# Kernel optimization log

Measured on AMD Instinct MI355X. Metric: run time of the kernel, lower is better.

The kernel has to match this reference:

```python
import jax, jax.numpy as jnp
import numpy as np

N_NODES = 40000
N_EDGES = 640000
IN, HID, OUT = 128, 128, 47


def setup_inputs() -> dict:
    key = jax.random.key(0)
    ks = jax.random.split(key, 12)
    def glorot(k, shape):
        fan = sum(shape)
        return jax.random.normal(k, shape, dtype=jnp.float32) * jnp.sqrt(2.0 / fan)
    return {
        "x": jax.random.normal(ks[0], (N_NODES, IN), dtype=jnp.float32),
        "src": jax.random.randint(ks[1], (N_EDGES,), 0, N_NODES),
        "dst": jax.random.randint(ks[2], (N_EDGES,), 0, N_NODES),
        "W_self0": glorot(ks[3], (IN, HID)),
        "W_neigh0": glorot(ks[4], (IN, HID)),
        "b0": jnp.zeros((HID,), dtype=jnp.float32),
        "W_self1": glorot(ks[5], (HID, HID)),
        "W_neigh1": glorot(ks[6], (HID, HID)),
        "b1": jnp.zeros((HID,), dtype=jnp.float32),
        "W_self2": glorot(ks[7], (HID, OUT)),
        "W_neigh2": glorot(ks[8], (HID, OUT)),
        "b2": jnp.zeros((OUT,), dtype=jnp.float32),
    }


def _sage_conv(h, src, dst, W_self, W_neigh, b):
    # DGL SAGEConv('mean'): mean of neighbor (src) feats scattered to dst,
    # then fc_neigh(h_neigh) + fc_self(h_self) + bias.
    n = h.shape[0]
    deg = jax.ops.segment_sum(jnp.ones_like(dst, dtype=h.dtype), dst, num_segments=n)
    agg = jax.ops.segment_sum(h[src], dst, num_segments=n)          # [N, d] gather + scatter-add
    h_neigh = agg / jnp.maximum(deg, 1.0)[:, None]                   # isolated nodes -> 0 (DGL behavior)
    return h @ W_self + h_neigh @ W_neigh + b


def reference(x, src, dst, W_self0, W_neigh0, b0, W_self1, W_neigh1, b1,
              W_self2, W_neigh2, b2):
    # Dropout is identity in eval mode; omitted here.
    h = _sage_conv(x, src, dst, W_self0, W_neigh0, b0)
    h = jax.nn.relu(h)
    h = _sage_conv(h, src, dst, W_self1, W_neigh1, b1)
    h = jax.nn.relu(h)
    h = _sage_conv(h, src, dst, W_self2, W_neigh2, b2)
    return h
```

## Files before the change

### kernel.cpp

```cpp
#include <hip/hip_runtime.h>
#include <hip/hip_bf16.h>
#include <stdint.h>

#define NN 40000
#define NE 640000
#define NB 157

typedef __attribute__((ext_vector_type(8))) short bf16x8;
typedef __attribute__((ext_vector_type(4))) float f32x4;
typedef __attribute__((ext_vector_type(2))) float f32x2v;

static __device__ __forceinline__ unsigned short f2b(float f) {
    unsigned b = __float_as_uint(f);
    return (unsigned short)((b + 0x7FFFu + ((b >> 16) & 1u)) >> 16);
}
static __device__ __forceinline__ float blo(unsigned v) { return __uint_as_float(v << 16); }
static __device__ __forceinline__ float bhi(unsigned v) { return __uint_as_float(v & 0xffff0000u); }

static __device__ __forceinline__ void acc4(float* a, uint2 v) {
    a[0] += blo(v.x); a[1] += bhi(v.x);
    a[2] += blo(v.y); a[3] += bhi(v.y);
}


#if __has_builtin(__builtin_amdgcn_cvt_pk_fp8_f32) && __has_builtin(__builtin_amdgcn_cvt_pk_f32_fp8)
#define FP8_HW 1
#else
#define FP8_HW 0
#endif

static __device__ __forceinline__ unsigned char f2fp8_sw(float f) {
    f = fminf(fmaxf(f, -448.f), 448.f);
    unsigned b = __float_as_uint(f);
    unsigned s = (b >> 24) & 0x80u;
    unsigned ab = b & 0x7fffffffu;
    if (ab < 0x3c000000u) return (unsigned char)s;
    unsigned r = ab + 0x7ffffu + ((ab >> 20) & 1u);
    unsigned e = ((r >> 23) - 120u) & 0xfu;
    unsigned m = (r >> 20) & 7u;
    return (unsigned char)(s | (e << 3) | m);
}
static __device__ __forceinline__ float fp82f_sw(unsigned char u) {
    unsigned s = ((unsigned)u & 0x80u) << 24;
    unsigned e = (u >> 3) & 15u, m = u & 7u;
    float nrm = __uint_as_float(s | ((e + 120u) << 23) | (m << 20));
    float dnm = __uint_as_float(s | 0x3f800000u) * (float)m * 0.001953125f;
    return e ? nrm : dnm;
}

static __device__ __forceinline__ unsigned pack_fp8x4(float a, float b, float c, float d) {
#if FP8_HW
    int v = __builtin_amdgcn_cvt_pk_fp8_f32(a, b, 0, false);
    v = __builtin_amdgcn_cvt_pk_fp8_f32(c, d, v, true);
    return (unsigned)v;
#else
    return (unsigned)f2fp8_sw(a) | ((unsigned)f2fp8_sw(b) << 8) |
           ((unsigned)f2fp8_sw(c) << 16) | ((unsigned)f2fp8_sw(d) << 24);
#endif
}

static __device__ __forceinline__ void acc4f8(float* a, unsigned v) {
#if FP8_HW
    f32x2v p0 = __builtin_amdgcn_cvt_pk_f32_fp8((int)v, false);
    f32x2v p1 = __builtin_amdgcn_cvt_pk_f32_fp8((int)v, true);
    a[0] += p0.x; a[1] += p0.y; a[2] += p1.x; a[3] += p1.y;
#else
    a[0] += fp82f_sw(v & 0xff);         a[1] += fp82f_sw((v >> 8) & 0xff);
    a[2] += fp82f_sw((v >> 16) & 0xff); a[3] += fp82f_sw(v >> 24);
#endif
}
static __device__ __forceinline__ void acc16f8(float* a, uint4 v) {
    acc4f8(a, v.x); acc4f8(a + 4, v.y); acc4f8(a + 8, v.z); acc4f8(a + 12, v.w);
}


__global__ __launch_bounds__(256) void scan1_kernel(const int* __restrict__ deg,
                                                    int* __restrict__ bsum) {
    int i = blockIdx.x * 256 + threadIdx.x;
    int v = (i < NN) ? deg[i] : 0;
#pragma unroll
    for (int off = 1; off < 64; off <<= 1) v += __shfl_xor(v, off);
    __shared__ int ws4[4];
    if ((threadIdx.x & 63) == 0) ws4[threadIdx.x >> 6] = v;
    __syncthreads();
    if (threadIdx.x == 0) bsum[blockIdx.x] = ws4[0] + ws4[1] + ws4[2] + ws4[3];
}

__global__ void scan_top_kernel(const int* __restrict__ bsum, int* __restrict__ btop) {
    int lane = threadIdx.x;
    int run = 0;
    for (int base = 0; base < NB; base += 64) {
        int idx = base + lane;
        int v = (idx < NB) ? bsum[idx] : 0;
        int s = v;
#pragma unroll
        for (int off = 1; off < 64; off <<= 1) { int t = __shfl_up(s, off); if (lane >= off) s += t; }
        if (idx < NB) btop[idx] = run + s - v;
        run += __shfl(s, 63);
    }
}

__global__ __launch_bounds__(256) void scan2_kernel(const int* __restrict__ deg,
                                                    const int* __restrict__ btop,
                                                    int* __restrict__ row_ptr) {
    int b = blockIdx.x;
    int i = b * 256 + threadIdx.x;
    int lane = threadIdx.x & 63, wv = threadIdx.x >> 6;
    int v = (i < NN) ? deg[i] : 0;
    int s = v;
#pragma unroll
    for (int off = 1; off < 64; off <<= 1) { int t = __shfl_up(s, off); if (lane >= off) s += t; }
    __shared__ int wsum[4];
    if (lane == 63) wsum[wv] = s;
    __syncthreads();
    int add = btop[b];
    for (int w = 0; w < wv; ++w) add += wsum[w];
    if (i < NN) row_ptr[i] = add + s - v;
    if (i == NN - 1) row_ptr[NN] = add + s;
}

__global__ void fill_csr_kernel(const int* __restrict__ src, const int* __restrict__ dst,
                                const int* __restrict__ row_ptr, int* __restrict__ cursor,
                                int* __restrict__ csr, int n) {
    int i = blockIdx.x * blockDim.x + threadIdx.x;
    if (i < n) {
        int d = dst[i];
        int pos = row_ptr[d] + atomicAdd(&cursor[d], 1);
        csr[pos] = src[i];
    }
}


__global__ __launch_bounds__(256) void prep_kernel(
    const float* __restrict__ x, const int* __restrict__ dst,
    const float* __restrict__ Ws0, const float* __restrict__ Wn0,
    const float* __restrict__ Ws1, const float* __restrict__ Wn1,
    const float* __restrict__ Ws2, const float* __restrict__ Wn2,
    int* __restrict__ deg, unsigned short* __restrict__ X,
    unsigned char* __restrict__ X8, unsigned char* __restrict__ H18,
    unsigned short* __restrict__ Hn,
    unsigned short* __restrict__ Wt0, unsigned short* __restrict__ Wt1,
    unsigned short* __restrict__ Wt2s, unsigned short* __restrict__ Wt2n) {
    int b = blockIdx.x, tid = threadIdx.x;
    if (b < 2500) {
        int i = b * 256 + tid;
        atomicAdd(&deg[dst[i]], 1);
    } else if (b < 7500) {
        int i = (b - 2500) * 256 + tid;
        int e = i << 2;
        float4 v = *(const float4*)(x + e);
        uint2 o;
        o.x = f2b(v.x) | ((unsigned)f2b(v.y) << 16);
        o.y = f2b(v.z) | ((unsigned)f2b(v.w) << 16);
        *(uint2*)(X + e) = o;
        *(unsigned*)(X8 + e) = pack_fp8x4(v.x, v.y, v.z, v.w);
    } else if (b < 7804) {
        int i = (b - 7500) * 256 + tid;
        if (i < 65536) {
            int l = i >> 15, j = i & 32767;
            int n = j >> 8, k = j & 255;
            const float* Ws = l ? Ws1 : Ws0;
            const float* Wn = l ? Wn1 : Wn0;
            float v = (k < 128) ? Ws[k * 128 + n] : Wn[(k - 128) * 128 + n];
            (l ? Wt1 : Wt0)[n * 256 + k] = f2b(v);
        } else if (i < 65536 + 6144) {
            int j = i - 65536;
            int n = j >> 7, k = j & 127;
            float v = (n < 47) ? Ws2[k * 47 + n] : 0.f;
            Wt2s[n * 128 + k] = f2b(v);
        } else {
            int j = i - 65536 - 6144;
            int n = j >> 7, k = j & 127;
            float v = (n < 47) ? Wn2[k * 47 + n] : 0.f;
            Wt2n[n * 128 + k] = f2b(v);
        }
    } else {
        if (tid < 16) *(uint2*)(X8 + (size_t)NN * 128 + tid * 8) = (uint2){0, 0};
        else if (tid < 32) *(uint2*)(H18 + (size_t)NN * 128 + (tid - 16) * 8) = (uint2){0, 0};
        else if (tid < 48) *(uint2*)((unsigned char*)(Hn + (size_t)NN * 64) + (tid - 32) * 8) = (uint2){0, 0};
    }
}


template <bool RELU, bool WFP8>
__global__ __launch_bounds__(256) void sage_layer_kernel(
    const unsigned short* __restrict__ Hin, const unsigned char* __restrict__ H8in,
    const int* __restrict__ csr, const int* __restrict__ row_ptr,
    const unsigned short* __restrict__ Wt, const float* __restrict__ bias,
    unsigned short* __restrict__ Hout, unsigned char* __restrict__ H8out) {
    __shared__ unsigned short agg_lds[16 * 128];

    int tid = threadIdx.x;
    int wv = tid >> 6, lane = tid & 63;
    int lr = lane & 15, lg = lane >> 4;
    int lr8 = lane & 7, g = lane >> 3;
    int t = g >> 1, sub = g & 1;
    int m0 = blockIdx.x * 16;

    bf16x8 afr[8];
#pragma unroll
    for (int kt = 0; kt < 4; ++kt)
        afr[kt] = *(const bf16x8*)(Hin + (size_t)(m0 + lr) * 128 + kt * 32 + lg * 8);

    int nb = m0 + wv * 4;
    int rp5 = (lane < 5) ? row_ptr[nb + lane] : 0;
    int beg = __shfl(rp5, t), end = __shfl(rp5, t + 1);
    int deg = end - beg;
    int half = (deg + 1) >> 1;
    int js = beg + sub * half;
    int je = sub ? end : beg + half;
    int last = (je > js) ? je - 1 : js;

    float a[16] = {};
    for (int j = js; j < je; j += 8) {
        int idxs[8];
#pragma unroll
        for (int k = 0; k < 8; ++k) idxs[k] = csr[min(j + k, last)];
#pragma unroll
        for (int k = 0; k < 8; ++k)
            if (j + k >= je) idxs[k] = NN;
        uint4 v[8];
#pragma unroll
        for (int k = 0; k < 8; ++k)
            v[k] = *(const uint4*)(H8in + (size_t)idxs[k] * 128 + lr8 * 16);
#pragma unroll
        for (int k = 0; k < 8; ++k) acc16f8(a, v[k]);
    }
#pragma unroll
    for (int k = 0; k < 16; ++k) a[k] += __shfl_xor(a[k], 8);

    if (sub == 0) {
        float inv = 1.0f / fmaxf((float)deg, 1.0f);
        uint4 o0, o1;
        o0.x = f2b(a[0] * inv)  | ((unsigned)f2b(a[1] * inv) << 16);
        o0.y = f2b(a[2] * inv)  | ((unsigned)f2b(a[3] * inv) << 16);
        o0.z = f2b(a[4] * inv)  | ((unsigned)f2b(a[5] * inv) << 16);
        o0.w = f2b(a[6] * inv)  | ((unsigned)f2b(a[7] * inv) << 16);
        o1.x = f2b(a[8] * inv)  | ((unsigned)f2b(a[9] * inv) << 16);
        o1.y = f2b(a[10] * inv) | ((unsigned)f2b(a[11] * inv) << 16);
        o1.z = f2b(a[12] * inv) | ((unsigned)f2b(a[13] * inv) << 16);
        o1.w = f2b(a[14] * inv) | ((unsigned)f2b(a[15] * inv) << 16);
        int row = wv * 4 + t;
        *(uint4*)&agg_lds[row * 128 + ((2 * lr8) ^ row) * 8] = o0;
        *(uint4*)&agg_lds[row * 128 + ((2 * lr8 + 1) ^ row) * 8] = o1;
    }
    __syncthreads();

#pragma unroll
    for (int kt = 0; kt < 4; ++kt) {
        int chunk = (kt * 4 + lg) ^ lr;
        afr[4 + kt] = *(const bf16x8*)&agg_lds[lr * 128 + chunk * 8];
    }

    int n0 = (wv * 2) * 16 + lr;
    int n1 = n0 + 16;
    f32x4 acc0 = (f32x4){0.f, 0.f, 0.f, 0.f};
    f32x4 acc1 = (f32x4){0.f, 0.f, 0.f, 0.f};
#pragma unroll
    for (int kt = 0; kt < 8; ++kt) {
        bf16x8 b0 = *(const bf16x8*)(Wt + (size_t)n0 * 256 + kt * 32 + lg * 8);
        bf16x8 b1 = *(const bf16x8*)(Wt + (size_t)n1 * 256 + kt * 32 + lg * 8);
        acc0 = __builtin_amdgcn_mfma_f32_16x16x32_bf16(afr[kt], b0, acc0, 0, 0, 0);
        acc1 = __builtin_amdgcn_mfma_f32_16x16x32_bf16(afr[kt], b1, acc1, 0, 0, 0);
    }

    float bs0 = bias[n0], bs1 = bias[n1];
#pragma unroll
    for (int r = 0; r < 4; ++r) {
        int m = m0 + lg * 4 + r;
        float v0 = acc0[r] + bs0;
        float v1 = acc1[r] + bs1;
        if (RELU) { v0 = fmaxf(v0, 0.f); v1 = fmaxf(v1, 0.f); }
        Hout[(size_t)m * 128 + n0] = f2b(v0);
        Hout[(size_t)m * 128 + n1] = f2b(v1);
        if (WFP8) {
#if FP8_HW
            H8out[(size_t)m * 128 + n0] =
                (unsigned char)(__builtin_amdgcn_cvt_pk_fp8_f32(v0, v0, 0, false) & 0xff);
            H8out[(size_t)m * 128 + n1] =
                (unsigned char)(__builtin_amdgcn_cvt_pk_fp8_f32(v1, v1, 0, false) & 0xff);
#else
            H8out[(size_t)m * 128 + n0] = f2fp8_sw(v0);
            H8out[(size_t)m * 128 + n1] = f2fp8_sw(v1);
#endif
        }
    }
}


__global__ __launch_bounds__(192) void dual_gemm_kernel(
    const unsigned short* __restrict__ H2,
    const unsigned short* __restrict__ Wt2s, const unsigned short* __restrict__ Wt2n,
    const float* __restrict__ b2,
    float* __restrict__ out, unsigned short* __restrict__ Hn) {
    int wv = threadIdx.x >> 6, lane = threadIdx.x & 63;
    int lr = lane & 15, lg = lane >> 4;

    bf16x8 bfr[2][4];
    float bs[2];
#pragma unroll
    for (int c = 0; c < 2; ++c) {
        int t = wv * 2 + c;
        bool is_s = t < 3;
        int n = (is_s ? t : t - 3) * 16 + lr;
        const unsigned short* W = is_s ? Wt2s : Wt2n;
#pragma unroll
        for (int kt = 0; kt < 4; ++kt)
            bfr[c][kt] = *(const bf16x8*)(W + (size_t)n * 128 + kt * 32 + lg * 8);
        bs[c] = (is_s && n < 47) ? b2[n] : 0.f;
    }

    for (int tt = 0; tt < 2; ++tt) {
        int m0 = blockIdx.x * 32 + tt * 16;
        bf16x8 afr[4];
#pragma unroll
        for (int kt = 0; kt < 4; ++kt)
            afr[kt] = *(const bf16x8*)(H2 + (size_t)(m0 + lr) * 128 + kt * 32 + lg * 8);
        f32x4 acc[2];
#pragma unroll
        for (int c = 0; c < 2; ++c) acc[c] = (f32x4){0.f, 0.f, 0.f, 0.f};
#pragma unroll
        for (int kt = 0; kt < 4; ++kt)
#pragma unroll
            for (int c = 0; c < 2; ++c)
                acc[c] = __builtin_amdgcn_mfma_f32_16x16x32_bf16(afr[kt], bfr[c][kt], acc[c], 0, 0, 0);
#pragma unroll
        for (int c = 0; c < 2; ++c) {
            int t = wv * 2 + c;
            bool is_s = t < 3;
            int n = (is_s ? t : t - 3) * 16 + lr;
#pragma unroll
            for (int r = 0; r < 4; ++r) {
                int m = m0 + lg * 4 + r;
                float v = acc[c][r] + bs[c];
                if (is_s) {
                    if (n < 47) out[(size_t)m * 47 + n] = v;
                } else {
                    Hn[(size_t)m * 64 + n] = f2b(v);
                }
            }
        }
    }
}


__global__ __launch_bounds__(256) void aggregate_out_kernel(
    const unsigned short* __restrict__ Hn, const int* __restrict__ csr,
    const int* __restrict__ row_ptr, float* __restrict__ out) {
    int wave = (blockIdx.x * blockDim.x + threadIdx.x) >> 6;
    int lane = threadIdx.x & 63;
    int nb = wave * 2;
    if (nb >= NN) return;
    int t = lane >> 5, sub = (lane >> 4) & 1, lc = lane & 15;
    int rp3 = (lane < 3) ? row_ptr[nb + lane] : 0;
    int beg = __shfl(rp3, t), end = __shfl(rp3, t + 1);
    int deg = end - beg;
    int half = (deg + 1) >> 1;
    int js = beg + sub * half;
    int je = sub ? end : beg + half;
    int last = (je > js) ? je - 1 : js;

    float a[4] = {};
    for (int j = js; j < je; j += 8) {
        int idxs[8];
#pragma unroll
        for (int k = 0; k < 8; ++k) idxs[k] = csr[min(j + k, last)];
#pragma unroll
        for (int k = 0; k < 8; ++k)
            if (j + k >= je) idxs[k] = NN;
        uint2 v[8];
#pragma unroll
        for (int k = 0; k < 8; ++k)
            v[k] = *(const uint2*)(Hn + (size_t)idxs[k] * 64 + lc * 4);
#pragma unroll
        for (int k = 0; k < 8; ++k) acc4(a, v[k]);
    }
#pragma unroll
    for (int k = 0; k < 4; ++k) a[k] += __shfl_xor(a[k], 16);

    if (sub == 0 && lc < 12) {
        float inv = 1.0f / fmaxf((float)deg, 1.0f);
        int node = nb + t;
        int c0 = lc * 4;
#pragma unroll
        for (int r = 0; r < 4; ++r)
            if (c0 + r < 47) out[(size_t)node * 47 + c0 + r] += a[r] * inv;
    }
}


extern "C" void kernel_launch(void* const* d_in, const int* in_sizes, int n_in,
                              void* d_out, int out_size, void* d_ws, size_t ws_size,
                              hipStream_t stream) {
    const float* x   = (const float*)d_in[0];
    const int*   src = (const int*)d_in[1];
    const int*   dst = (const int*)d_in[2];
    const float* Ws0 = (const float*)d_in[3];
    const float* Wn0 = (const float*)d_in[4];
    const float* b0  = (const float*)d_in[5];
    const float* Ws1 = (const float*)d_in[6];
    const float* Wn1 = (const float*)d_in[7];
    const float* b1  = (const float*)d_in[8];
    const float* Ws2 = (const float*)d_in[9];
    const float* Wn2 = (const float*)d_in[10];
    const float* b2  = (const float*)d_in[11];
    float* out = (float*)d_out;

    uintptr_t p = ((uintptr_t)d_ws + 255) & ~(uintptr_t)255;
    auto take = [&](size_t bytes) {
        void* r = (void*)p;
        p = (p + bytes + 255) & ~(uintptr_t)255;
        return r;
    };
    int* deg     = (int*)take(40000 * 4);
    int* cursor  = (int*)take(40000 * 4);
    int* row_ptr = (int*)take(40004 * 4);
    int* csr     = (int*)take(640000 * 4);
    unsigned short* X   = (unsigned short*)take((size_t)NN * 128 * 2);
    unsigned short* H1  = (unsigned short*)take((size_t)NN * 128 * 2);
    unsigned short* H2  = X;
    unsigned short* Wt0 = (unsigned short*)take(128 * 256 * 2);
    unsigned short* Wt1 = (unsigned short*)take(128 * 256 * 2);
    unsigned short* Wt2s = (unsigned short*)take(48 * 128 * 2);
    unsigned short* Wt2n = (unsigned short*)take(48 * 128 * 2);
    unsigned short* Hn  = (unsigned short*)take((size_t)(NN + 1) * 64 * 2);
    int* bsum = (int*)take(NB * 4);
    int* btop = (int*)take(NB * 4);
    unsigned char* X8  = (unsigned char*)take((size_t)(NN + 1) * 128);
    unsigned char* H18 = (unsigned char*)take((size_t)(NN + 1) * 128);

    hipMemsetAsync(deg, 0, 80000 * sizeof(int), stream);
    prep_kernel<<<7805, 256, 0, stream>>>(x, dst, Ws0, Wn0, Ws1, Wn1, Ws2, Wn2,
                                          deg, X, X8, H18, Hn, Wt0, Wt1, Wt2s, Wt2n);
    scan1_kernel<<<NB, 256, 0, stream>>>(deg, bsum);
    scan_top_kernel<<<1, 64, 0, stream>>>(bsum, btop);
    scan2_kernel<<<NB, 256, 0, stream>>>(deg, btop, row_ptr);
    fill_csr_kernel<<<2500, 256, 0, stream>>>(src, dst, row_ptr, cursor, csr, NE);

    sage_layer_kernel<true, true><<<2500, 256, 0, stream>>>(X, X8, csr, row_ptr, Wt0, b0, H1, H18);
    sage_layer_kernel<true, false><<<2500, 256, 0, stream>>>(H1, H18, csr, row_ptr, Wt1, b1, H2, nullptr);
    dual_gemm_kernel<<<1250, 192, 0, stream>>>(H2, Wt2s, Wt2n, b2, out, Hn);
    aggregate_out_kernel<<<5000, 256, 0, stream>>>(Hn, csr, row_ptr, out);
}
```

Measured before the change: 180.1 us.

## Split feature tables into column slabs and separate aggregation from GEMM

Stores the fp8 feature tables as two 64-column slabs and the final-layer neighbor projections as 32- and 16-column slabs. Aggregation runs in column-split passes so each gather pass works on a smaller table that fits better in cache. It also splits the fused aggregate+GEMM layer kernel into a separate gather kernel and a GEMM kernel that keeps weights in registers, and folds the scan-top step into scan2. The cost is more kernel launches, repeated CSR traversal per slab, and an extra bf16 agg buffer written to and read back from memory.

```diff
diff --git a/kernel.cpp b/kernel.cpp
--- a/kernel.cpp
+++ b/kernel.cpp
@@ -5,10 +5,12 @@
 #define NN 40000
 #define NE 640000
 #define NB 157
+#define SUB8 ((size_t)(NN + 1) * 64)
 
 typedef __attribute__((ext_vector_type(8))) short bf16x8;
 typedef __attribute__((ext_vector_type(4))) float f32x4;
 typedef __attribute__((ext_vector_type(2))) float f32x2v;
+typedef __attribute__((ext_vector_type(4))) unsigned u32x4;
 
 static __device__ __forceinline__ unsigned short f2b(float f) {
     unsigned b = __float_as_uint(f);
@@ -17,6 +19,12 @@
 static __device__ __forceinline__ float blo(unsigned v) { return __uint_as_float(v << 16); }
 static __device__ __forceinline__ float bhi(unsigned v) { return __uint_as_float(v & 0xffff0000u); }
 
+static __device__ __forceinline__ void acc8(float* a, uint4 v) {
+    a[0] += blo(v.x); a[1] += bhi(v.x);
+    a[2] += blo(v.y); a[3] += bhi(v.y);
+    a[4] += blo(v.z); a[5] += bhi(v.z);
+    a[6] += blo(v.w); a[7] += bhi(v.w);
+}
 static __device__ __forceinline__ void acc4(float* a, uint2 v) {
     a[0] += blo(v.x); a[1] += bhi(v.x);
     a[2] += blo(v.y); a[3] += bhi(v.y);
@@ -58,6 +66,13 @@
            ((unsigned)f2fp8_sw(c) << 16) | ((unsigned)f2fp8_sw(d) << 24);
 #endif
 }
+static __device__ __forceinline__ unsigned char f2fp8(float v) {
+#if FP8_HW
+    return (unsigned char)(__builtin_amdgcn_cvt_pk_fp8_f32(v, v, 0, false) & 0xff);
+#else
+    return f2fp8_sw(v);
+#endif
+}
 
 static __device__ __forceinline__ void acc4f8(float* a, unsigned v) {
 #if FP8_HW
@@ -86,34 +101,28 @@
     if (threadIdx.x == 0) bsum[blockIdx.x] = ws4[0] + ws4[1] + ws4[2] + ws4[3];
 }
 
-__global__ void scan_top_kernel(const int* __restrict__ bsum, int* __restrict__ btop) {
-    int lane = threadIdx.x;
-    int run = 0;
-    for (int base = 0; base < NB; base += 64) {
-        int idx = base + lane;
-        int v = (idx < NB) ? bsum[idx] : 0;
-        int s = v;
-#pragma unroll
-        for (int off = 1; off < 64; off <<= 1) { int t = __shfl_up(s, off); if (lane >= off) s += t; }
-        if (idx < NB) btop[idx] = run + s - v;
-        run += __shfl(s, 63);
-    }
-}
-
 __global__ __launch_bounds__(256) void scan2_kernel(const int* __restrict__ deg,
-                                                    const int* __restrict__ btop,
+                                                    const int* __restrict__ bsum,
                                                     int* __restrict__ row_ptr) {
     int b = blockIdx.x;
-    int i = b * 256 + threadIdx.x;
-    int lane = threadIdx.x & 63, wv = threadIdx.x >> 6;
+    int tid = threadIdx.x, lane = tid & 63, wv = tid >> 6;
+    __shared__ int base_s;
+    __shared__ int wsum[4];
+    if (tid < 64) {
+        int s = 0;
+        for (int idx = tid; idx < b; idx += 64) s += bsum[idx];
+#pragma unroll
+        for (int off = 1; off < 64; off <<= 1) s += __shfl_xor(s, off);
+        if (tid == 0) base_s = s;
+    }
+    int i = b * 256 + tid;
     int v = (i < NN) ? deg[i] : 0;
     int s = v;
 #pragma unroll
     for (int off = 1; off < 64; off <<= 1) { int t = __shfl_up(s, off); if (lane >= off) s += t; }
-    __shared__ int wsum[4];
     if (lane == 63) wsum[wv] = s;
     __syncthreads();
-    int add = btop[b];
+    int add = base_s;
     for (int w = 0; w < wv; ++w) add += wsum[w];
     if (i < NN) row_ptr[i] = add + s - v;
     if (i == NN - 1) row_ptr[NN] = add + s;
@@ -138,7 +147,7 @@
     const float* __restrict__ Ws2, const float* __restrict__ Wn2,
     int* __restrict__ deg, unsigned short* __restrict__ X,
     unsigned char* __restrict__ X8, unsigned char* __restrict__ H18,
-    unsigned short* __restrict__ Hn,
+    unsigned short* __restrict__ HnA, unsigned short* __restrict__ HnB,
     unsigned short* __restrict__ Wt0, unsigned short* __restrict__ Wt1,
     unsigned short* __restrict__ Wt2s, unsigned short* __restrict__ Wt2n) {
     int b = blockIdx.x, tid = threadIdx.x;
@@ -148,12 +157,15 @@
     } else if (b < 7500) {
         int i = (b - 2500) * 256 + tid;
         int e = i << 2;
+        int node = e >> 7, col = e & 127;
         float4 v = *(const float4*)(x + e);
         uint2 o;
         o.x = f2b(v.x) | ((unsigned)f2b(v.y) << 16);
         o.y = f2b(v.z) | ((unsigned)f2b(v.w) << 16);
         *(uint2*)(X + e) = o;
-        *(unsigned*)(X8 + e) = pack_fp8x4(v.x, v.y, v.z, v.w);
+        int c = col >> 6, co = col & 63;
+        *(unsigned*)(X8 + (size_t)c * SUB8 + (size_t)node * 64 + co) =
+            pack_fp8x4(v.x, v.y, v.z, v.w);
     } else if (b < 7804) {
         int i = (b - 7500) * 256 + tid;
         if (i < 65536) {
@@ -175,63 +187,56 @@
             Wt2n[n * 128 + k] = f2b(v);
         }
     } else {
-        if (tid < 16) *(uint2*)(X8 + (size_t)NN * 128 + tid * 8) = (uint2){0, 0};
-        else if (tid < 32) *(uint2*)(H18 + (size_t)NN * 128 + (tid - 16) * 8) = (uint2){0, 0};
-        else if (tid < 48) *(uint2*)((unsigned char*)(Hn + (size_t)NN * 64) + (tid - 32) * 8) = (uint2){0, 0};
-    }
-}
-
-
-template <bool RELU, bool WFP8>
-__global__ __launch_bounds__(256) void sage_layer_kernel(
-    const unsigned short* __restrict__ Hin, const unsigned char* __restrict__ H8in,
-    const int* __restrict__ csr, const int* __restrict__ row_ptr,
-    const unsigned short* __restrict__ Wt, const float* __restrict__ bias,
-    unsigned short* __restrict__ Hout, unsigned char* __restrict__ H8out) {
-    __shared__ unsigned short agg_lds[16 * 128];
-
+        if (tid < 8)       *(uint2*)(X8 + (size_t)NN * 64 + tid * 8) = (uint2){0, 0};
+        else if (tid < 16) *(uint2*)(X8 + SUB8 + (size_t)NN * 64 + (tid - 8) * 8) = (uint2){0, 0};
+        else if (tid < 24) *(uint2*)(H18 + (size_t)NN * 64 + (tid - 16) * 8) = (uint2){0, 0};
+        else if (tid < 32) *(uint2*)(H18 + SUB8 + (size_t)NN * 64 + (tid - 24) * 8) = (uint2){0, 0};
+        else if (tid < 40) *(uint2*)((unsigned char*)(HnA + (size_t)NN * 32) + (tid - 32) * 8) = (uint2){0, 0};
+        else if (tid < 44) *(uint2*)((unsigned char*)(HnB + (size_t)NN * 16) + (tid - 40) * 8) = (uint2){0, 0};
+    }
+}
+
+
+__global__ __launch_bounds__(256) void agg8_kernel(
+    const unsigned char* __restrict__ T, const int* __restrict__ csr,
+    const int* __restrict__ row_ptr, unsigned short* __restrict__ agg, int col0) {
     int tid = threadIdx.x;
     int wv = tid >> 6, lane = tid & 63;
-    int lr = lane & 15, lg = lane >> 4;
-    int lr8 = lane & 7, g = lane >> 3;
-    int t = g >> 1, sub = g & 1;
-    int m0 = blockIdx.x * 16;
-
-    bf16x8 afr[8];
-#pragma unroll
-    for (int kt = 0; kt < 4; ++kt)
-        afr[kt] = *(const bf16x8*)(Hin + (size_t)(m0 + lr) * 128 + kt * 32 + lg * 8);
-
-    int nb = m0 + wv * 4;
+    int lr4 = lane & 3, g = lane >> 2;
+    int t = g >> 2, q = g & 3;
+    int nb = blockIdx.x * 16 + wv * 4;
+
     int rp5 = (lane < 5) ? row_ptr[nb + lane] : 0;
     int beg = __shfl(rp5, t), end = __shfl(rp5, t + 1);
     int deg = end - beg;
-    int half = (deg + 1) >> 1;
-    int js = beg + sub * half;
-    int je = sub ? end : beg + half;
+    int qlen = (deg + 3) >> 2;
+    int js = beg + q * qlen;
+    int je = min(js + qlen, end);
     int last = (je > js) ? je - 1 : js;
 
     float a[16] = {};
-    for (int j = js; j < je; j += 8) {
-        int idxs[8];
-#pragma unroll
-        for (int k = 0; k < 8; ++k) idxs[k] = csr[min(j + k, last)];
-#pragma unroll
-        for (int k = 0; k < 8; ++k)
+    for (int j = js; j < je; j += 4) {
+        int idxs[4];
+#pragma unroll
+        for (int k = 0; k < 4; ++k) idxs[k] = __builtin_nontemporal_load(csr + min(j + k, last));
+#pragma unroll
+        for (int k = 0; k < 4; ++k)
             if (j + k >= je) idxs[k] = NN;
-        uint4 v[8];
-#pragma unroll
-        for (int k = 0; k < 8; ++k)
-            v[k] = *(const uint4*)(H8in + (size_t)idxs[k] * 128 + lr8 * 16);
-#pragma unroll
-        for (int k = 0; k < 8; ++k) acc16f8(a, v[k]);
-    }
-#pragma unroll
-    for (int k = 0; k < 16; ++k) a[k] += __shfl_xor(a[k], 8);
-
-    if (sub == 0) {
+        uint4 v[4];
+#pragma unroll
+        for (int k = 0; k < 4; ++k)
+            v[k] = *(const uint4*)(T + (size_t)idxs[k] * 64 + lr4 * 16);
+#pragma unroll
+        for (int k = 0; k < 4; ++k) acc16f8(a, v[k]);
+    }
+#pragma unroll
+    for (int k = 0; k < 16; ++k) {
+        a[k] += __shfl_xor(a[k], 4);
+        a[k] += __shfl_xor(a[k], 8);
+    }
+    if (q == 0) {
         float inv = 1.0f / fmaxf((float)deg, 1.0f);
-        uint4 o0, o1;
+        u32x4 o0, o1;
         o0.x = f2b(a[0] * inv)  | ((unsigned)f2b(a[1] * inv) << 16);
         o0.y = f2b(a[2] * inv)  | ((unsigned)f2b(a[3] * inv) << 16);
         o0.z = f2b(a[4] * inv)  | ((unsigned)f2b(a[5] * inv) << 16);
@@ -240,49 +245,67 @@
         o1.y = f2b(a[10] * inv) | ((unsigned)f2b(a[11] * inv) << 16);
         o1.z = f2b(a[12] * inv) | ((unsigned)f2b(a[13] * inv) << 16);
         o1.w = f2b(a[14] * inv) | ((unsigned)f2b(a[15] * inv) << 16);
-        int row = wv * 4 + t;
-        *(uint4*)&agg_lds[row * 128 + ((2 * lr8) ^ row) * 8] = o0;
-        *(uint4*)&agg_lds[row * 128 + ((2 * lr8 + 1) ^ row) * 8] = o1;
-    }
-    __syncthreads();
-
-#pragma unroll
-    for (int kt = 0; kt < 4; ++kt) {
-        int chunk = (kt * 4 + lg) ^ lr;
-        afr[4 + kt] = *(const bf16x8*)&agg_lds[lr * 128 + chunk * 8];
-    }
-
-    int n0 = (wv * 2) * 16 + lr;
-    int n1 = n0 + 16;
-    f32x4 acc0 = (f32x4){0.f, 0.f, 0.f, 0.f};
-    f32x4 acc1 = (f32x4){0.f, 0.f, 0.f, 0.f};
-#pragma unroll
-    for (int kt = 0; kt < 8; ++kt) {
-        bf16x8 b0 = *(const bf16x8*)(Wt + (size_t)n0 * 256 + kt * 32 + lg * 8);
-        bf16x8 b1 = *(const bf16x8*)(Wt + (size_t)n1 * 256 + kt * 32 + lg * 8);
-        acc0 = __builtin_amdgcn_mfma_f32_16x16x32_bf16(afr[kt], b0, acc0, 0, 0, 0);
-        acc1 = __builtin_amdgcn_mfma_f32_16x16x32_bf16(afr[kt], b1, acc1, 0, 0, 0);
-    }
-
-    float bs0 = bias[n0], bs1 = bias[n1];
-#pragma unroll
-    for (int r = 0; r < 4; ++r) {
-        int m = m0 + lg * 4 + r;
-        float v0 = acc0[r] + bs0;
-        float v1 = acc1[r] + bs1;
-        if (RELU) { v0 = fmaxf(v0, 0.f); v1 = fmaxf(v1, 0.f); }
-        Hout[(size_t)m * 128 + n0] = f2b(v0);
-        Hout[(size_t)m * 128 + n1] = f2b(v1);
-        if (WFP8) {
-#if FP8_HW
-            H8out[(size_t)m * 128 + n0] =
-                (unsigned char)(__builtin_amdgcn_cvt_pk_fp8_f32(v0, v0, 0, false) & 0xff);
-            H8out[(size_t)m * 128 + n1] =
-                (unsigned char)(__builtin_amdgcn_cvt_pk_fp8_f32(v1, v1, 0, false) & 0xff);
-#else
-            H8out[(size_t)m * 128 + n0] = f2fp8_sw(v0);
-            H8out[(size_t)m * 128 + n1] = f2fp8_sw(v1);
-#endif
+        int node = nb + t;
+        u32x4* dstp = (u32x4*)(agg + (size_t)node * 128 + col0 + lr4 * 16);
+        __builtin_nontemporal_store(o0, dstp);
+        __builtin_nontemporal_store(o1, dstp + 1);
+    }
+}
+
+
+template <bool RELU, bool WFP8>
+__global__ __launch_bounds__(256) void gemm_layer_kernel(
+    const unsigned short* __restrict__ Hin, const unsigned short* __restrict__ agg,
+    const unsigned short* __restrict__ Wt, const float* __restrict__ bias,
+    unsigned short* __restrict__ Hout, unsigned char* __restrict__ H8out, int tpb) {
+    int wv = threadIdx.x >> 6, lane = threadIdx.x & 63;
+    int lr = lane & 15, lg = lane >> 4;
+
+    bf16x8 bfr[2][8];
+    float bs[2];
+#pragma unroll
+    for (int c = 0; c < 2; ++c) {
+        int n = (wv * 2 + c) * 16 + lr;
+#pragma unroll
+        for (int kt = 0; kt < 8; ++kt)
+            bfr[c][kt] = *(const bf16x8*)(Wt + (size_t)n * 256 + kt * 32 + lg * 8);
+        bs[c] = bias[n];
+    }
+
+    for (int tt = 0; tt < tpb; ++tt) {
+        int m0 = (blockIdx.x * tpb + tt) * 16;
+        bf16x8 afr[8];
+#pragma unroll
+        for (int kt = 0; kt < 4; ++kt)
+            afr[kt] = __builtin_nontemporal_load(
+                (const bf16x8*)(Hin + (size_t)(m0 + lr) * 128 + kt * 32 + lg * 8));
+#pragma unroll
+        for (int kt = 0; kt < 4; ++kt)
+            afr[4 + kt] = __builtin_nontemporal_load(
+                (const bf16x8*)(agg + (size_t)(m0 + lr) * 128 + kt * 32 + lg * 8));
+        f32x4 acc0 = (f32x4){0.f, 0.f, 0.f, 0.f};
+        f32x4 acc1 = (f32x4){0.f, 0.f, 0.f, 0.f};
+#pragma unroll
+        for (int kt = 0; kt < 8; ++kt) {
+            acc0 = __builtin_amdgcn_mfma_f32_16x16x32_bf16(afr[kt], bfr[0][kt], acc0, 0, 0, 0);
+            acc1 = __builtin_amdgcn_mfma_f32_16x16x32_bf16(afr[kt], bfr[1][kt], acc1, 0, 0, 0);
+        }
+        int n0 = (wv * 2) * 16 + lr;
+        int n1 = n0 + 16;
+        int sub = wv >> 1;
+#pragma unroll
+        for (int r = 0; r < 4; ++r) {
+            int m = m0 + lg * 4 + r;
+            float v0 = acc0[r] + bs[0];
+            float v1 = acc1[r] + bs[1];
+            if (RELU) { v0 = fmaxf(v0, 0.f); v1 = fmaxf(v1, 0.f); }
+            Hout[(size_t)m * 128 + n0] = f2b(v0);
+            Hout[(size_t)m * 128 + n1] = f2b(v1);
+            if (WFP8) {
+                unsigned char* hb = H8out + (size_t)sub * SUB8 + (size_t)m * 64;
+                hb[n0 & 63] = f2fp8(v0);
+                hb[n1 & 63] = f2fp8(v1);
+            }
         }
     }
 }
@@ -291,8 +314,8 @@
 __global__ __launch_bounds__(192) void dual_gemm_kernel(
     const unsigned short* __restrict__ H2,
     const unsigned short* __restrict__ Wt2s, const unsigned short* __restrict__ Wt2n,
-    const float* __restrict__ b2,
-    float* __restrict__ out, unsigned short* __restrict__ Hn) {
+    const float* __restrict__ b2, float* __restrict__ out,
+    unsigned short* __restrict__ HnA, unsigned short* __restrict__ HnB) {
     int wv = threadIdx.x >> 6, lane = threadIdx.x & 63;
     int lr = lane & 15, lg = lane >> 4;
 
@@ -315,7 +338,8 @@
         bf16x8 afr[4];
 #pragma unroll
         for (int kt = 0; kt < 4; ++kt)
-            afr[kt] = *(const bf16x8*)(H2 + (size_t)(m0 + lr) * 128 + kt * 32 + lg * 8);
+            afr[kt] = __builtin_nontemporal_load(
+                (const bf16x8*)(H2 + (size_t)(m0 + lr) * 128 + kt * 32 + lg * 8));
         f32x4 acc[2];
 #pragma unroll
         for (int c = 0; c < 2; ++c) acc[c] = (f32x4){0.f, 0.f, 0.f, 0.f};
@@ -336,7 +360,8 @@
                 if (is_s) {
                     if (n < 47) out[(size_t)m * 47 + n] = v;
                 } else {
-                    Hn[(size_t)m * 64 + n] = f2b(v);
+                    if (n < 32) HnA[(size_t)m * 32 + n] = f2b(v);
+                    else        HnB[(size_t)m * 16 + (n - 32)] = f2b(v);
                 }
             }
         }
@@ -344,47 +369,95 @@
 }
 
 
-__global__ __launch_bounds__(256) void aggregate_out_kernel(
-    const unsigned short* __restrict__ Hn, const int* __restrict__ csr,
+__global__ __launch_bounds__(256) void aggoutA_kernel(
+    const unsigned short* __restrict__ T, const int* __restrict__ csr,
     const int* __restrict__ row_ptr, float* __restrict__ out) {
-    int wave = (blockIdx.x * blockDim.x + threadIdx.x) >> 6;
-    int lane = threadIdx.x & 63;
-    int nb = wave * 2;
-    if (nb >= NN) return;
-    int t = lane >> 5, sub = (lane >> 4) & 1, lc = lane & 15;
-    int rp3 = (lane < 3) ? row_ptr[nb + lane] : 0;
-    int beg = __shfl(rp3, t), end = __shfl(rp3, t + 1);
+    int tid = threadIdx.x;
+    int wv = tid >> 6, lane = tid & 63;
+    int lr4 = lane & 3, g = lane >> 2;
+    int t = g >> 2, q = g & 3;
+    int nb = blockIdx.x * 16 + wv * 4;
+    int rp5 = (lane < 5) ? row_ptr[nb + lane] : 0;
+    int beg = __shfl(rp5, t), end = __shfl(rp5, t + 1);
     int deg = end - beg;
-    int half = (deg + 1) >> 1;
-    int js = beg + sub * half;
-    int je = sub ? end : beg + half;
+    int qlen = (deg + 3) >> 2;
+    int js = beg + q * qlen;
+    int je = min(js + qlen, end);
     int last = (je > js) ? je - 1 : js;
 
-    float a[4] = {};
-    for (int j = js; j < je; j += 8) {
-        int idxs[8];
-#pragma unroll
-        for (int k = 0; k < 8; ++k) idxs[k] = csr[min(j + k, last)];
-#pragma unroll
-        for (int k = 0; k < 8; ++k)
+    float a[8] = {};
+    for (int j = js; j < je; j += 4) {
+        int idxs[4];
+#pragma unroll
+        for (int k = 0; k < 4; ++k) idxs[k] = __builtin_nontemporal_load(csr + min(j + k, last));
+#pragma unroll
+        for (int k = 0; k < 4; ++k)
             if (j + k >= je) idxs[k] = NN;
-        uint2 v[8];
-#pragma unroll
-        for (int k = 0; k < 8; ++k)
-            v[k] = *(const uint2*)(Hn + (size_t)idxs[k] * 64 + lc * 4);
-#pragma unroll
-        for (int k = 0; k < 8; ++k) acc4(a, v[k]);
-    }
-#pragma unroll
-    for (int k = 0; k < 4; ++k) a[k] += __shfl_xor(a[k], 16);
-
-    if (sub == 0 && lc < 12) {
+        uint4 v[4];
+#pragma unroll
+        for (int k = 0; k < 4; ++k)
+            v[k] = *(const uint4*)(T + (size_t)idxs[k] * 32 + lr4 * 8);
+#pragma unroll
+        for (int k = 0; k < 4; ++k) acc8(a, v[k]);
+    }
+#pragma unroll
+    for (int k = 0; k < 8; ++k) {
+        a[k] += __shfl_xor(a[k], 4);
+        a[k] += __shfl_xor(a[k], 8);
+    }
+    if (q == 0) {
         float inv = 1.0f / fmaxf((float)deg, 1.0f);
         int node = nb + t;
-        int c0 = lc * 4;
-#pragma unroll
-        for (int r = 0; r < 4; ++r)
-            if (c0 + r < 47) out[(size_t)node * 47 + c0 + r] += a[r] * inv;
+#pragma unroll
+        for (int r = 0; r < 8; ++r)
+            out[(size_t)node * 47 + lr4 * 8 + r] += a[r] * inv;
+    }
+}
+
+__global__ __launch_bounds__(256) void aggoutB_kernel(
+    const unsigned short* __restrict__ T, const int* __restrict__ csr,
+    const int* __restrict__ row_ptr, float* __restrict__ out) {
+    int tid = threadIdx.x;
+    int wv = tid >> 6, lane = tid & 63;
+    int lr4 = lane & 3, g = lane >> 2;
+    int t = g >> 2, q = g & 3;
+    int nb = blockIdx.x * 16 + wv * 4;
+    int rp5 = (lane < 5) ? row_ptr[nb + lane] : 0;
+    int beg = __shfl(rp5, t), end = __shfl(rp5, t + 1);
+    int deg = end - beg;
+    int qlen = (deg + 3) >> 2;
+    int js = beg + q * qlen;
+    int je = min(js + qlen, end);
+    int last = (je > js) ? je - 1 : js;
+
+    float a[4] = {};
+    for (int j = js; j < je; j += 4) {
+        int idxs[4];
+#pragma unroll
+        for (int k = 0; k < 4; ++k) idxs[k] = __builtin_nontemporal_load(csr + min(j + k, last));
+#pragma unroll
+        for (int k = 0; k < 4; ++k)
+            if (j + k >= je) idxs[k] = NN;
+        uint2 v[4];
+#pragma unroll
+        for (int k = 0; k < 4; ++k)
+            v[k] = *(const uint2*)(T + (size_t)idxs[k] * 16 + lr4 * 4);
+#pragma unroll
+        for (int k = 0; k < 4; ++k) acc4(a, v[k]);
+    }
+#pragma unroll
+    for (int k = 0; k < 4; ++k) {
+        a[k] += __shfl_xor(a[k], 4);
+        a[k] += __shfl_xor(a[k], 8);
+    }
+    if (q == 0) {
+        float inv = 1.0f / fmaxf((float)deg, 1.0f);
+        int node = nb + t;
+#pragma unroll
+        for (int r = 0; r < 4; ++r) {
+            int col = 32 + lr4 * 4 + r;
+            if (col < 47) out[(size_t)node * 47 + col] += a[r] * inv;
+        }
     }
 }
 
@@ -419,26 +492,31 @@
     unsigned short* X   = (unsigned short*)take((size_t)NN * 128 * 2);
     unsigned short* H1  = (unsigned short*)take((size_t)NN * 128 * 2);
     unsigned short* H2  = X;
+    unsigned short* agg = (unsigned short*)take((size_t)NN * 128 * 2);
     unsigned short* Wt0 = (unsigned short*)take(128 * 256 * 2);
     unsigned short* Wt1 = (unsigned short*)take(128 * 256 * 2);
     unsigned short* Wt2s = (unsigned short*)take(48 * 128 * 2);
     unsigned short* Wt2n = (unsigned short*)take(48 * 128 * 2);
-    unsigned short* Hn  = (unsigned short*)take((size_t)(NN + 1) * 64 * 2);
+    unsigned short* HnA = (unsigned short*)take((size_t)(NN + 1) * 32 * 2);
+    unsigned short* HnB = (unsigned short*)take((size_t)(NN + 1) * 16 * 2);
     int* bsum = (int*)take(NB * 4);
-    int* btop = (int*)take(NB * 4);
-    unsigned char* X8  = (unsigned char*)take((size_t)(NN + 1) * 128);
-    unsigned char* H18 = (unsigned char*)take((size_t)(NN + 1) * 128);
-
-    hipMemsetAsync(deg, 0, 80000 * sizeof(int), stream);
+    unsigned char* X8  = (unsigned char*)take(2 * SUB8);
+    unsigned char* H18 = (unsigned char*)take(2 * SUB8);
+
+    (void)hipMemsetAsync(deg, 0, 80000 * sizeof(int), stream);
     prep_kernel<<<7805, 256, 0, stream>>>(x, dst, Ws0, Wn0, Ws1, Wn1, Ws2, Wn2,
-                                          deg, X, X8, H18, Hn, Wt0, Wt1, Wt2s, Wt2n);
+                                          deg, X, X8, H18, HnA, HnB, Wt0, Wt1, Wt2s, Wt2n);
     scan1_kernel<<<NB, 256, 0, stream>>>(deg, bsum);
-    scan_top_kernel<<<1, 64, 0, stream>>>(bsum, btop);
-    scan2_kernel<<<NB, 256, 0, stream>>>(deg, btop, row_ptr);
+    scan2_kernel<<<NB, 256, 0, stream>>>(deg, bsum, row_ptr);
     fill_csr_kernel<<<2500, 256, 0, stream>>>(src, dst, row_ptr, cursor, csr, NE);
 
-    sage_layer_kernel<true, true><<<2500, 256, 0, stream>>>(X, X8, csr, row_ptr, Wt0, b0, H1, H18);
-    sage_layer_kernel<true, false><<<2500, 256, 0, stream>>>(H1, H18, csr, row_ptr, Wt1, b1, H2, nullptr);
-    dual_gemm_kernel<<<1250, 192, 0, stream>>>(H2, Wt2s, Wt2n, b2, out, Hn);
-    aggregate_out_kernel<<<5000, 256, 0, stream>>>(Hn, csr, row_ptr, out);
-}
+    agg8_kernel<<<2500, 256, 0, stream>>>(X8, csr, row_ptr, agg, 0);
+    agg8_kernel<<<2500, 256, 0, stream>>>(X8 + SUB8, csr, row_ptr, agg, 64);
+    gemm_layer_kernel<true, true><<<1250, 256, 0, stream>>>(X, agg, Wt0, b0, H1, H18, 2);
+    agg8_kernel<<<2500, 256, 0, stream>>>(H18, csr, row_ptr, agg, 0);
+    agg8_kernel<<<2500, 256, 0, stream>>>(H18 + SUB8, csr, row_ptr, agg, 64);
+    gemm_layer_kernel<true, false><<<1250, 256, 0, stream>>>(H1, agg, Wt1, b1, H2, nullptr, 2);
+    dual_gemm_kernel<<<1250, 192, 0, stream>>>(H2, Wt2s, Wt2n, b2, out, HnA, HnB);
+    aggoutA_kernel<<<2500, 256, 0, stream>>>(HnA, csr, row_ptr, out);
+    aggoutB_kernel<<<2500, 256, 0, stream>>>(HnB, csr, row_ptr, out);
+}
```

Result: slower. 209.3 us (+16.2%).
